# Kernel tuning notes

Measured on AMD Instinct MI355X. Metric: run time of the kernel, lower is better.

Reference implementation:

```python
import jax, jax.numpy as jnp
import numpy as np

B, H, S, D = 2, 16, 2048, 64

def setup_inputs() -> dict:
    key = jax.random.key(0)
    kq, kk, kv, km = jax.random.split(key, 4)
    q = jax.random.normal(kq, (B, H, S, D), dtype=jnp.float32)
    k = jax.random.normal(kk, (B, H, S, D), dtype=jnp.float32)
    v = jax.random.normal(kv, (B, H, S, D), dtype=jnp.float32)
    mask = jax.random.randint(km, (B, 1, S, S), 0, 2, dtype=jnp.int32)
    return {"q": q, "k": k, "v": v, "mask": mask}

def reference(q, k, v, mask):
    d_model = q.shape[-1]
    # scores: [B, H, S, S]
    score = jnp.einsum('bhqd,bhkd->bhqk', q, k) / jnp.sqrt(jnp.float32(d_model))
    score = jnp.where(mask == 0, jnp.float32(-1e9), score)
    attn = jax.nn.softmax(score, axis=-1)
    return jnp.einsum('bhqk,bhkd->bhqd', attn, v)
```

## Files before the change

### kernel.cpp

```cpp
#include <hip/hip_runtime.h>
#include <hip/hip_bf16.h>


#define B_ 2
#define H_ 16
#define S_ 2048
#define D_ 64
#define BQ 128
#define BK 64
#define NT (S_ / BK)
#define PADW 72
#define TILEB (BK * D_ * 2)

typedef __attribute__((ext_vector_type(4))) float f32x4;
typedef __attribute__((ext_vector_type(8))) short bf16x8;
typedef __attribute__((ext_vector_type(4))) short bf16x4;
typedef __attribute__((ext_vector_type(4))) unsigned u32x4;

#define QSCALE 0.1803368801111137f
#define MASKNEG (-1.4426950408889634e9f)

static __device__ __forceinline__ short f2bf(float f) {
  __hip_bfloat16 h = __float2bfloat16(f);
  short s; __builtin_memcpy(&s, &h, sizeof(s)); return s;
}
static __device__ __forceinline__ float fexp2(float x) {
  return __builtin_amdgcn_exp2f(x);
}
static __device__ __forceinline__ unsigned cvt_pk_bf16(float a, float b) {
  unsigned r;
  asm("v_cvt_pk_bf16_f32 %0, %1, %2" : "=v"(r) : "v"(a), "v"(b));
  return r;
}
static __device__ __forceinline__ void gload_lds16(const void* g, void* l) {
  __builtin_amdgcn_global_load_lds(
      (__attribute__((address_space(1))) void*)g,
      (__attribute__((address_space(3))) void*)l, 16, 0, 0);
}
static __device__ __forceinline__ void perm32sw(unsigned& a, unsigned& b) {
  asm("v_permlane32_swap_b32 %0, %1" : "+v"(a), "+v"(b));
}
static __device__ __forceinline__ void perm16sw(unsigned& a, unsigned& b) {
  asm("v_permlane16_swap_b32 %0, %1" : "+v"(a), "+v"(b));
}

__global__ __launch_bounds__(256)
void pack_all(const float* __restrict__ kg, const float* __restrict__ vg,
              const int* __restrict__ mg,
              short* __restrict__ kw, short* __restrict__ vw,
              unsigned long long* __restrict__ mwp) {
  __shared__ float sv[BK][D_ + 1];
  const int bx  = blockIdx.x;
  const int tid = threadIdx.x;

  if (bx < 1024) {
    const int t  = bx & 31;
    const int bh = bx >> 5;
    const float* kt = kg + ((size_t)bh * S_ + t * BK) * D_;
    const float* vt = vg + ((size_t)bh * S_ + t * BK) * D_;
    short* ko = kw + ((size_t)bh * NT + t) * (BK * D_);
    short* vo = vw + ((size_t)bh * NT + t) * (BK * D_);

    const int row = tid >> 2;
    const int swz = (row & 7) << 4;

    #pragma unroll
    for (int c = 0; c < 2; ++c) {
      const int x = (tid & 3) * 32 + c * 16;
      const int dsrc = (x ^ swz) >> 1;
      const float4 u0 = *(const float4*)(kt + row * D_ + dsrc);
      const float4 u1 = *(const float4*)(kt + row * D_ + dsrc + 4);
      uint4 w;
      w.x = cvt_pk_bf16(u0.x, u0.y); w.y = cvt_pk_bf16(u0.z, u0.w);
      w.z = cvt_pk_bf16(u1.x, u1.y); w.w = cvt_pk_bf16(u1.z, u1.w);
      *(uint4*)(ko + row * D_ + (x >> 1)) = w;
    }

    #pragma unroll
    for (int i = 0; i < 4; ++i) {
      const int id = tid + 256 * i;
      const int r = id >> 4, c4 = (id & 15) * 4;
      const float4 u = *(const float4*)(vt + r * D_ + c4);
      sv[r][c4] = u.x; sv[r][c4+1] = u.y; sv[r][c4+2] = u.z; sv[r][c4+3] = u.w;
    }
    __syncthreads();
    #pragma unroll
    for (int c = 0; c < 2; ++c) {
      const int x = (tid & 3) * 32 + c * 16;
      const int ksrc = (x ^ swz) >> 1;
      uint4 w;
      w.x = cvt_pk_bf16(sv[ksrc+0][row], sv[ksrc+1][row]);
      w.y = cvt_pk_bf16(sv[ksrc+2][row], sv[ksrc+3][row]);
      w.z = cvt_pk_bf16(sv[ksrc+4][row], sv[ksrc+5][row]);
      w.w = cvt_pk_bf16(sv[ksrc+6][row], sv[ksrc+7][row]);
      *(uint4*)(vo + row * D_ + (x >> 1)) = w;
    }
  } else {
    const int r4   = bx - 1024;
    const int wv   = tid >> 6;
    const int lane = tid & 63;
    const int row  = r4 * 4 + wv;
    const int* mr = mg + (size_t)row * S_;
    unsigned long long* out = mwp + (size_t)row * NT;
    #pragma unroll
    for (int g = 0; g < 8; ++g) {
      const int4 v = *(const int4*)(mr + g * 256 + lane * 4);
      const unsigned long long b0 = __ballot(v.x != 0);
      const unsigned long long b1 = __ballot(v.y != 0);
      const unsigned long long b2 = __ballot(v.z != 0);
      const unsigned long long b3 = __ballot(v.w != 0);
      if (lane < 4) {
        const int tl = lane;
        const unsigned long long u =
            ((b0 >> (16 * tl)) & 0xFFFFULL)
          | (((b1 >> (16 * tl)) & 0xFFFFULL) << 16)
          | (((b2 >> (16 * tl)) & 0xFFFFULL) << 32)
          | (((b3 >> (16 * tl)) & 0xFFFFULL) << 48);
        out[g * 4 + tl] = u;
      }
    }
  }
}

__global__ __launch_bounds__(512, 8)
void attn_main(const float* __restrict__ qg, const short* __restrict__ kw,
               const short* __restrict__ vw,
               const unsigned long long* __restrict__ mw,
               float* __restrict__ outg) {
  __shared__ short sKV[2][2][BK * D_];

  const int tid  = threadIdx.x;
  const int lane = tid & 63;
  const int wv   = tid >> 6;
  const int l15  = lane & 15;
  const int quad = lane >> 4;

  const int f  = blockIdx.y * 16 + blockIdx.x;
  const int nf = (f & 7) * 64 + (f >> 3);
  const int bh = nf >> 4;
  const int b  = bh >> 4;
  const int q0 = (nf & 15) * BQ;
  const int qw = q0 + wv * 16 + l15;

  bf16x8 qf[2];
  {
    const float* qrow = qg + ((size_t)bh * S_ + qw) * D_;
    #pragma unroll
    for (int ks = 0; ks < 2; ++ks) {
      const float4 u0 = *(const float4*)(qrow + ks*32 + quad*8);
      const float4 u1 = *(const float4*)(qrow + ks*32 + quad*8 + 4);
      bf16x8 fq;
      fq[0]=f2bf(u0.x*QSCALE); fq[1]=f2bf(u0.y*QSCALE);
      fq[2]=f2bf(u0.z*QSCALE); fq[3]=f2bf(u0.w*QSCALE);
      fq[4]=f2bf(u1.x*QSCALE); fq[5]=f2bf(u1.y*QSCALE);
      fq[6]=f2bf(u1.z*QSCALE); fq[7]=f2bf(u1.w*QSCALE);
      qf[ks] = fq;
    }
  }

  bf16x8 onesf;
  #pragma unroll
  for (int j = 0; j < 8; ++j) onesf[j] = (short)0x3F80;

  f32x4 O[4];
  #pragma unroll
  for (int dt = 0; dt < 4; ++dt) O[dt] = (f32x4){0.f, 0.f, 0.f, 0.f};
  f32x4 Ol = (f32x4){0.f, 0.f, 0.f, 0.f};

  const char* kt = (const char*)(kw + (size_t)bh * NT * BK * D_);
  const char* vt = (const char*)(vw + (size_t)bh * NT * BK * D_);
  const unsigned long long* mb = mw + ((size_t)b * S_ + qw) * NT;
  const int so = tid * 16;

  const int swz = (l15 & 7) << 4;
  const int ro0 = l15*128 + (( 0 + quad*16) ^ swz);
  const int ro1 = l15*128 + ((64 + quad*16) ^ swz);

  gload_lds16(kt + so, (char*)sKV + so);
  gload_lds16(vt + so, (char*)sKV + 8192 + so);
  kt += TILEB; vt += TILEB;
  int cur = 0;
  __syncthreads();

  for (int t = 0; t < NT; ++t) {
    const unsigned long long m64 = mb[t];
    if (t < NT - 1) {
      const int nb = (cur ^ 1) << 14;
      gload_lds16(kt + so, (char*)sKV + nb + so);
      gload_lds16(vt + so, (char*)sKV + nb + 8192 + so);
      kt += TILEB; vt += TILEB;
    }
    const char* kb = (const char*)sKV + (cur << 14);
    const char* vb = kb + 8192;

    f32x4 st[4];
    __builtin_amdgcn_s_setprio(1);
    #pragma unroll
    for (int mt = 0; mt < 4; ++mt) {
      f32x4 acc = (f32x4){0.f, 0.f, 0.f, 0.f};
      const bf16x8 kf0 = *(const bf16x8*)(kb + mt*2048 + ro0);
      const bf16x8 kf1 = *(const bf16x8*)(kb + mt*2048 + ro1);
      acc = __builtin_amdgcn_mfma_f32_16x16x32_bf16(kf0, qf[0], acc, 0, 0, 0);
      acc = __builtin_amdgcn_mfma_f32_16x16x32_bf16(kf1, qf[1], acc, 0, 0, 0);
      st[mt] = acc;
    }
    __builtin_amdgcn_s_setprio(0);

    const unsigned xlo = ((unsigned)m64) >> quad;
    const unsigned xhi = ((unsigned)(m64 >> 32)) >> quad;
    uint2 U[4];
    #pragma unroll
    for (int mt = 0; mt < 4; ++mt) {
      float p0 = fexp2(st[mt].x);
      float p1 = fexp2(st[mt].y);
      float p2 = fexp2(st[mt].z);
      float p3 = fexp2(st[mt].w);
      const int a0 = __builtin_amdgcn_sbfe((int)xlo, mt*4,      1);
      const int a1 = __builtin_amdgcn_sbfe((int)xlo, mt*4 + 16, 1);
      const int a2 = __builtin_amdgcn_sbfe((int)xhi, mt*4,      1);
      const int a3 = __builtin_amdgcn_sbfe((int)xhi, mt*4 + 16, 1);
      p0 = __uint_as_float(__float_as_uint(p0) & (unsigned)a0);
      p1 = __uint_as_float(__float_as_uint(p1) & (unsigned)a1);
      p2 = __uint_as_float(__float_as_uint(p2) & (unsigned)a2);
      p3 = __uint_as_float(__float_as_uint(p3) & (unsigned)a3);
      U[mt].x = cvt_pk_bf16(p0, p1);
      U[mt].y = cvt_pk_bf16(p2, p3);
    }

    unsigned w00 = U[0].x, w02 = U[1].x;
    perm32sw(w00, w02); perm16sw(w00, w02);
    unsigned w01 = U[0].y, w03 = U[1].y;
    perm32sw(w01, w03); perm16sw(w01, w03);
    unsigned w10 = U[2].x, w12 = U[3].x;
    perm32sw(w10, w12); perm16sw(w10, w12);
    unsigned w11 = U[2].y, w13 = U[3].y;
    perm32sw(w11, w13); perm16sw(w11, w13);
    bf16x8 pf0, pf1;
    {
      u32x4 t0 = (u32x4){w00, w01, w02, w03};
      u32x4 t1 = (u32x4){w10, w11, w12, w13};
      __builtin_memcpy(&pf0, &t0, 16);
      __builtin_memcpy(&pf1, &t1, 16);
    }

    __builtin_amdgcn_s_setprio(1);
    #pragma unroll
    for (int dt = 0; dt < 4; ++dt) {
      const bf16x8 vf0 = *(const bf16x8*)(vb + dt*2048 + ro0);
      const bf16x8 vf1 = *(const bf16x8*)(vb + dt*2048 + ro1);
      O[dt] = __builtin_amdgcn_mfma_f32_16x16x32_bf16(pf0, vf0, O[dt], 0, 0, 0);
      O[dt] = __builtin_amdgcn_mfma_f32_16x16x32_bf16(pf1, vf1, O[dt], 0, 0, 0);
    }
    Ol = __builtin_amdgcn_mfma_f32_16x16x32_bf16(pf0, onesf, Ol, 0, 0, 0);
    Ol = __builtin_amdgcn_mfma_f32_16x16x32_bf16(pf1, onesf, Ol, 0, 0, 0);
    __builtin_amdgcn_s_setprio(0);

    __syncthreads();
    cur ^= 1;
  }

  float ir[4];
  ir[0] = 1.0f / Ol.x; ir[1] = 1.0f / Ol.y;
  ir[2] = 1.0f / Ol.z; ir[3] = 1.0f / Ol.w;

  float* ob = outg + ((size_t)bh * S_ + q0 + wv*16) * D_;
  #pragma unroll
  for (int dt = 0; dt < 4; ++dt) {
    ob[(quad*4 + 0)*D_ + dt*16 + l15] = O[dt].x * ir[0];
    ob[(quad*4 + 1)*D_ + dt*16 + l15] = O[dt].y * ir[1];
    ob[(quad*4 + 2)*D_ + dt*16 + l15] = O[dt].z * ir[2];
    ob[(quad*4 + 3)*D_ + dt*16 + l15] = O[dt].w * ir[3];
  }
}

__global__ __launch_bounds__(256, 4)
void attn_fallback(const float* __restrict__ qg, const float* __restrict__ kg,
                   const float* __restrict__ vg, const int* __restrict__ maskg,
                   float* __restrict__ outg) {
  __shared__ short sK[BK][PADW];
  __shared__ short sVT[D_][PADW];
  __shared__ short sP[4][16][PADW];

  const int tid  = threadIdx.x;
  const int lane = tid & 63;
  const int wv   = tid >> 6;
  const int l15  = lane & 15;
  const int quad = lane >> 4;

  const int bh = blockIdx.y;
  const int b  = bh >> 4;
  const int q0 = blockIdx.x * 64;
  const int qw = q0 + wv * 16 + l15;

  bf16x8 qf[2];
  {
    const float* qrow = qg + ((size_t)bh * S_ + qw) * D_;
    #pragma unroll
    for (int ks = 0; ks < 2; ++ks) {
      const float4 u0 = *(const float4*)(qrow + ks*32 + quad*8);
      const float4 u1 = *(const float4*)(qrow + ks*32 + quad*8 + 4);
      bf16x8 fq;
      fq[0]=f2bf(u0.x*QSCALE); fq[1]=f2bf(u0.y*QSCALE);
      fq[2]=f2bf(u0.z*QSCALE); fq[3]=f2bf(u0.w*QSCALE);
      fq[4]=f2bf(u1.x*QSCALE); fq[5]=f2bf(u1.y*QSCALE);
      fq[6]=f2bf(u1.z*QSCALE); fq[7]=f2bf(u1.w*QSCALE);
      qf[ks] = fq;
    }
  }

  f32x4 O[4];
  #pragma unroll
  for (int dt = 0; dt < 4; ++dt) O[dt] = (f32x4){0.f, 0.f, 0.f, 0.f};
  float m = -3.0e38f, l = 0.f;

  const float* kbase = kg + (size_t)bh * S_ * D_;
  const float* vbase = vg + (size_t)bh * S_ * D_;
  const int*   mrow  = maskg + ((size_t)b * S_ + qw) * S_;

  for (int t0 = 0; t0 < S_; t0 += BK) {
    __syncthreads();
    #pragma unroll
    for (int i = 0; i < 4; ++i) {
      const int id = tid + 256*i;
      const int key = id >> 4, d4 = (id & 15) * 4;
      const float4 u = *(const float4*)(kbase + (size_t)(t0 + key)*D_ + d4);
      bf16x4 w; w[0]=f2bf(u.x); w[1]=f2bf(u.y); w[2]=f2bf(u.z); w[3]=f2bf(u.w);
      *(bf16x4*)&sK[key][d4] = w;
    }
    #pragma unroll
    for (int i = 0; i < 2; ++i) {
      const int id = tid + 256*i;
      const int kp = id & 31, d4 = (id >> 5) * 4;
      const float4 a = *(const float4*)(vbase + (size_t)(t0 + 2*kp    )*D_ + d4);
      const float4 c = *(const float4*)(vbase + (size_t)(t0 + 2*kp + 1)*D_ + d4);
      const float av[4] = {a.x, a.y, a.z, a.w};
      const float cv[4] = {c.x, c.y, c.z, c.w};
      #pragma unroll
      for (int j = 0; j < 4; ++j) {
        const unsigned pk = (unsigned)(unsigned short)f2bf(av[j])
                          | ((unsigned)(unsigned short)f2bf(cv[j]) << 16);
        *(unsigned*)&sVT[d4 + j][2*kp] = pk;
      }
    }
    __syncthreads();

    int4 mk[4];
    #pragma unroll
    for (int mt = 0; mt < 4; ++mt)
      mk[mt] = *(const int4*)(mrow + t0 + mt*16 + quad*4);

    f32x4 st[4];
    #pragma unroll
    for (int mt = 0; mt < 4; ++mt) {
      f32x4 acc = (f32x4){0.f, 0.f, 0.f, 0.f};
      #pragma unroll
      for (int ks = 0; ks < 2; ++ks) {
        const bf16x8 kf = *(const bf16x8*)&sK[mt*16 + l15][ks*32 + quad*8];
        acc = __builtin_amdgcn_mfma_f32_16x16x32_bf16(kf, qf[ks], acc, 0, 0, 0);
      }
      st[mt] = acc;
    }

    float cmax = -3.0e38f;
    #pragma unroll
    for (int mt = 0; mt < 4; ++mt) {
      f32x4 s = st[mt];
      s.x = mk[mt].x ? s.x : MASKNEG;
      s.y = mk[mt].y ? s.y : MASKNEG;
      s.z = mk[mt].z ? s.z : MASKNEG;
      s.w = mk[mt].w ? s.w : MASKNEG;
      st[mt] = s;
      cmax = fmaxf(cmax, fmaxf(fmaxf(s.x, s.y), fmaxf(s.z, s.w)));
    }
    cmax = fmaxf(cmax, __shfl_xor(cmax, 16));
    cmax = fmaxf(cmax, __shfl_xor(cmax, 32));
    const float mnew  = fmaxf(m, cmax);
    const float alpha = fexp2(m - mnew);
    m = mnew;

    float lsum = 0.f;
    #pragma unroll
    for (int mt = 0; mt < 4; ++mt) {
      const float p0 = fexp2(st[mt].x - mnew);
      const float p1 = fexp2(st[mt].y - mnew);
      const float p2 = fexp2(st[mt].z - mnew);
      const float p3 = fexp2(st[mt].w - mnew);
      lsum += (p0 + p1) + (p2 + p3);
      bf16x4 pw; pw[0]=f2bf(p0); pw[1]=f2bf(p1); pw[2]=f2bf(p2); pw[3]=f2bf(p3);
      *(bf16x4*)&sP[wv][l15][mt*16 + quad*4] = pw;
    }
    lsum += __shfl_xor(lsum, 16);
    lsum += __shfl_xor(lsum, 32);
    l = l * alpha + lsum;

    const float ar0 = __shfl(alpha, quad*4 + 0);
    const float ar1 = __shfl(alpha, quad*4 + 1);
    const float ar2 = __shfl(alpha, quad*4 + 2);
    const float ar3 = __shfl(alpha, quad*4 + 3);
    #pragma unroll
    for (int dt = 0; dt < 4; ++dt) {
      O[dt].x *= ar0; O[dt].y *= ar1; O[dt].z *= ar2; O[dt].w *= ar3;
    }

    asm volatile("s_waitcnt lgkmcnt(0)" ::: "memory");

    const bf16x8 pf0 = *(const bf16x8*)&sP[wv][l15][quad*8];
    const bf16x8 pf1 = *(const bf16x8*)&sP[wv][l15][32 + quad*8];
    #pragma unroll
    for (int dt = 0; dt < 4; ++dt) {
      const bf16x8 vf0 = *(const bf16x8*)&sVT[dt*16 + l15][quad*8];
      const bf16x8 vf1 = *(const bf16x8*)&sVT[dt*16 + l15][32 + quad*8];
      O[dt] = __builtin_amdgcn_mfma_f32_16x16x32_bf16(pf0, vf0, O[dt], 0, 0, 0);
      O[dt] = __builtin_amdgcn_mfma_f32_16x16x32_bf16(pf1, vf1, O[dt], 0, 0, 0);
    }
  }

  float ir[4];
  #pragma unroll
  for (int r = 0; r < 4; ++r) ir[r] = 1.0f / __shfl(l, quad*4 + r);

  float* ob = outg + ((size_t)bh * S_ + q0 + wv*16) * D_;
  #pragma unroll
  for (int dt = 0; dt < 4; ++dt) {
    ob[(quad*4 + 0)*D_ + dt*16 + l15] = O[dt].x * ir[0];
    ob[(quad*4 + 1)*D_ + dt*16 + l15] = O[dt].y * ir[1];
    ob[(quad*4 + 2)*D_ + dt*16 + l15] = O[dt].z * ir[2];
    ob[(quad*4 + 3)*D_ + dt*16 + l15] = O[dt].w * ir[3];
  }
}

extern "C" void kernel_launch(void* const* d_in, const int* in_sizes, int n_in,
                              void* d_out, int out_size, void* d_ws, size_t ws_size,
                              hipStream_t stream) {
  const float* q    = (const float*)d_in[0];
  const float* k    = (const float*)d_in[1];
  const float* v    = (const float*)d_in[2];
  const int*   mask = (const int*)d_in[3];
  float* out = (float*)d_out;

  const size_t kvbytes = (size_t)B_ * H_ * S_ * D_ * 2;
  const size_t mbytes  = (size_t)B_ * S_ * NT * 8;
  const size_t need    = 2 * kvbytes + mbytes;

  if (d_ws != nullptr && ws_size >= need) {
    short* kwp = (short*)d_ws;
    short* vwp = (short*)((char*)d_ws + kvbytes);
    unsigned long long* mwp = (unsigned long long*)((char*)d_ws + 2 * kvbytes);
    pack_all<<<dim3(2048), 256, 0, stream>>>(k, v, mask, kwp, vwp, mwp);
    attn_main<<<dim3(S_ / BQ, B_ * H_), 512, 0, stream>>>(q, kwp, vwp, mwp, out);
  } else {
    attn_fallback<<<dim3(S_ / 64, B_ * H_), 256, 0, stream>>>(q, k, v, mask, out);
  }
}
```

Baseline: 169.5 us.

## Split KV range across two blocks and combine partial outputs

```diff
diff --git a/kernel.cpp b/kernel.cpp
--- a/kernel.cpp
+++ b/kernel.cpp
@@ -9,6 +9,7 @@
 #define BQ 128
 #define BK 64
 #define NT (S_ / BK)
+#define NTH (NT / 2)
 #define PADW 72
 #define TILEB (BK * D_ * 2)
 
@@ -123,10 +124,10 @@
 }
 
 __global__ __launch_bounds__(512, 8)
-void attn_main(const float* __restrict__ qg, const short* __restrict__ kw,
-               const short* __restrict__ vw,
-               const unsigned long long* __restrict__ mw,
-               float* __restrict__ outg) {
+void attn_split(const float* __restrict__ qg, const short* __restrict__ kw,
+                const short* __restrict__ vw,
+                const unsigned long long* __restrict__ mw,
+                float* __restrict__ Op, float* __restrict__ lw) {
   __shared__ short sKV[2][2][BK * D_];
 
   const int tid  = threadIdx.x;
@@ -135,12 +136,16 @@
   const int l15  = lane & 15;
   const int quad = lane >> 4;
 
-  const int f  = blockIdx.y * 16 + blockIdx.x;
-  const int nf = (f & 7) * 64 + (f >> 3);
-  const int bh = nf >> 4;
+  const int f  = blockIdx.y * 32 + blockIdx.x;
+  const int nf = (f & 7) * 128 + (f >> 3);
+  const int bh = nf >> 5;
   const int b  = bh >> 4;
-  const int q0 = (nf & 15) * BQ;
+  const int rest = nf & 31;
+  const int qb = rest >> 1;
+  const int sp = rest & 1;
+  const int q0 = qb * BQ;
   const int qw = q0 + wv * 16 + l15;
+  const int soff = sp * NTH;
 
   bf16x8 qf[2];
   {
@@ -167,9 +172,9 @@
   for (int dt = 0; dt < 4; ++dt) O[dt] = (f32x4){0.f, 0.f, 0.f, 0.f};
   f32x4 Ol = (f32x4){0.f, 0.f, 0.f, 0.f};
 
-  const char* kt = (const char*)(kw + (size_t)bh * NT * BK * D_);
-  const char* vt = (const char*)(vw + (size_t)bh * NT * BK * D_);
-  const unsigned long long* mb = mw + ((size_t)b * S_ + qw) * NT;
+  const char* kt = (const char*)(kw + ((size_t)bh * NT + soff) * BK * D_);
+  const char* vt = (const char*)(vw + ((size_t)bh * NT + soff) * BK * D_);
+  const unsigned long long* mb = mw + ((size_t)b * S_ + qw) * NT + soff;
   const int so = tid * 16;
 
   const int swz = (l15 & 7) << 4;
@@ -182,9 +187,9 @@
   int cur = 0;
   __syncthreads();
 
-  for (int t = 0; t < NT; ++t) {
+  for (int t = 0; t < NTH; ++t) {
     const unsigned long long m64 = mb[t];
-    if (t < NT - 1) {
+    if (t < NTH - 1) {
       const int nb = (cur ^ 1) << 14;
       gload_lds16(kt + so, (char*)sKV + nb + so);
       gload_lds16(vt + so, (char*)sKV + nb + 8192 + so);
@@ -259,6 +264,174 @@
     cur ^= 1;
   }
 
+  float* ob = Op + (((size_t)sp * 32 + bh) * S_ + q0 + wv*16) * D_;
+  #pragma unroll
+  for (int dt = 0; dt < 4; ++dt) {
+    ob[(quad*4 + 0)*D_ + dt*16 + l15] = O[dt].x;
+    ob[(quad*4 + 1)*D_ + dt*16 + l15] = O[dt].y;
+    ob[(quad*4 + 2)*D_ + dt*16 + l15] = O[dt].z;
+    ob[(quad*4 + 3)*D_ + dt*16 + l15] = O[dt].w;
+  }
+  if (l15 == 0) {
+    float* lb = lw + ((size_t)sp * 32 + bh) * S_ + q0 + wv*16 + quad*4;
+    lb[0] = Ol.x; lb[1] = Ol.y; lb[2] = Ol.z; lb[3] = Ol.w;
+  }
+}
+
+__global__ __launch_bounds__(256)
+void combine(const float* __restrict__ Op, const float* __restrict__ lw,
+             float* __restrict__ outg) {
+  const size_t OPHALF = (size_t)32 * S_ * D_;
+  const size_t LHALF  = (size_t)32 * S_;
+  const int gid = blockIdx.x * 256 + threadIdx.x;
+  const int r  = gid >> 4;
+  const int d4 = (gid & 15) * 4;
+  const float4 a = *(const float4*)(Op + (size_t)r * D_ + d4);
+  const float4 c = *(const float4*)(Op + OPHALF + (size_t)r * D_ + d4);
+  const float li = 1.0f / (lw[r] + lw[LHALF + r]);
+  float4 o;
+  o.x = (a.x + c.x) * li; o.y = (a.y + c.y) * li;
+  o.z = (a.z + c.z) * li; o.w = (a.w + c.w) * li;
+  *(float4*)(outg + (size_t)r * D_ + d4) = o;
+}
+
+__global__ __launch_bounds__(512, 8)
+void attn_main(const float* __restrict__ qg, const short* __restrict__ kw,
+               const short* __restrict__ vw,
+               const unsigned long long* __restrict__ mw,
+               float* __restrict__ outg) {
+  __shared__ short sKV[2][2][BK * D_];
+
+  const int tid  = threadIdx.x;
+  const int lane = tid & 63;
+  const int wv   = tid >> 6;
+  const int l15  = lane & 15;
+  const int quad = lane >> 4;
+
+  const int f  = blockIdx.y * 16 + blockIdx.x;
+  const int nf = (f & 7) * 64 + (f >> 3);
+  const int bh = nf >> 4;
+  const int b  = bh >> 4;
+  const int q0 = (nf & 15) * BQ;
+  const int qw = q0 + wv * 16 + l15;
+
+  bf16x8 qf[2];
+  {
+    const float* qrow = qg + ((size_t)bh * S_ + qw) * D_;
+    #pragma unroll
+    for (int ks = 0; ks < 2; ++ks) {
+      const float4 u0 = *(const float4*)(qrow + ks*32 + quad*8);
+      const float4 u1 = *(const float4*)(qrow + ks*32 + quad*8 + 4);
+      bf16x8 fq;
+      fq[0]=f2bf(u0.x*QSCALE); fq[1]=f2bf(u0.y*QSCALE);
+      fq[2]=f2bf(u0.z*QSCALE); fq[3]=f2bf(u0.w*QSCALE);
+      fq[4]=f2bf(u1.x*QSCALE); fq[5]=f2bf(u1.y*QSCALE);
+      fq[6]=f2bf(u1.z*QSCALE); fq[7]=f2bf(u1.w*QSCALE);
+      qf[ks] = fq;
+    }
+  }
+
+  bf16x8 onesf;
+  #pragma unroll
+  for (int j = 0; j < 8; ++j) onesf[j] = (short)0x3F80;
+
+  f32x4 O[4];
+  #pragma unroll
+  for (int dt = 0; dt < 4; ++dt) O[dt] = (f32x4){0.f, 0.f, 0.f, 0.f};
+  f32x4 Ol = (f32x4){0.f, 0.f, 0.f, 0.f};
+
+  const char* kt = (const char*)(kw + (size_t)bh * NT * BK * D_);
+  const char* vt = (const char*)(vw + (size_t)bh * NT * BK * D_);
+  const unsigned long long* mb = mw + ((size_t)b * S_ + qw) * NT;
+  const int so = tid * 16;
+
+  const int swz = (l15 & 7) << 4;
+  const int ro0 = l15*128 + (( 0 + quad*16) ^ swz);
+  const int ro1 = l15*128 + ((64 + quad*16) ^ swz);
+
+  gload_lds16(kt + so, (char*)sKV + so);
+  gload_lds16(vt + so, (char*)sKV + 8192 + so);
+  kt += TILEB; vt += TILEB;
+  int cur = 0;
+  __syncthreads();
+
+  for (int t = 0; t < NT; ++t) {
+    const unsigned long long m64 = mb[t];
+    if (t < NT - 1) {
+      const int nb = (cur ^ 1) << 14;
+      gload_lds16(kt + so, (char*)sKV + nb + so);
+      gload_lds16(vt + so, (char*)sKV + nb + 8192 + so);
+      kt += TILEB; vt += TILEB;
+    }
+    const char* kb = (const char*)sKV + (cur << 14);
+    const char* vb = kb + 8192;
+
+    f32x4 st[4];
+    __builtin_amdgcn_s_setprio(1);
+    #pragma unroll
+    for (int mt = 0; mt < 4; ++mt) {
+      f32x4 acc = (f32x4){0.f, 0.f, 0.f, 0.f};
+      const bf16x8 kf0 = *(const bf16x8*)(kb + mt*2048 + ro0);
+      const bf16x8 kf1 = *(const bf16x8*)(kb + mt*2048 + ro1);
+      acc = __builtin_amdgcn_mfma_f32_16x16x32_bf16(kf0, qf[0], acc, 0, 0, 0);
+      acc = __builtin_amdgcn_mfma_f32_16x16x32_bf16(kf1, qf[1], acc, 0, 0, 0);
+      st[mt] = acc;
+    }
+    __builtin_amdgcn_s_setprio(0);
+
+    const unsigned xlo = ((unsigned)m64) >> quad;
+    const unsigned xhi = ((unsigned)(m64 >> 32)) >> quad;
+    uint2 U[4];
+    #pragma unroll
+    for (int mt = 0; mt < 4; ++mt) {
+      float p0 = fexp2(st[mt].x);
+      float p1 = fexp2(st[mt].y);
+      float p2 = fexp2(st[mt].z);
+      float p3 = fexp2(st[mt].w);
+      const int a0 = __builtin_amdgcn_sbfe((int)xlo, mt*4,      1);
+      const int a1 = __builtin_amdgcn_sbfe((int)xlo, mt*4 + 16, 1);
+      const int a2 = __builtin_amdgcn_sbfe((int)xhi, mt*4,      1);
+      const int a3 = __builtin_amdgcn_sbfe((int)xhi, mt*4 + 16, 1);
+      p0 = __uint_as_float(__float_as_uint(p0) & (unsigned)a0);
+      p1 = __uint_as_float(__float_as_uint(p1) & (unsigned)a1);
+      p2 = __uint_as_float(__float_as_uint(p2) & (unsigned)a2);
+      p3 = __uint_as_float(__float_as_uint(p3) & (unsigned)a3);
+      U[mt].x = cvt_pk_bf16(p0, p1);
+      U[mt].y = cvt_pk_bf16(p2, p3);
+    }
+
+    unsigned w00 = U[0].x, w02 = U[1].x;
+    perm32sw(w00, w02); perm16sw(w00, w02);
+    unsigned w01 = U[0].y, w03 = U[1].y;
+    perm32sw(w01, w03); perm16sw(w01, w03);
+    unsigned w10 = U[2].x, w12 = U[3].x;
+    perm32sw(w10, w12); perm16sw(w10, w12);
+    unsigned w11 = U[2].y, w13 = U[3].y;
+    perm32sw(w11, w13); perm16sw(w11, w13);
+    bf16x8 pf0, pf1;
+    {
+      u32x4 t0 = (u32x4){w00, w01, w02, w03};
+      u32x4 t1 = (u32x4){w10, w11, w12, w13};
+      __builtin_memcpy(&pf0, &t0, 16);
+      __builtin_memcpy(&pf1, &t1, 16);
+    }
+
+    __builtin_amdgcn_s_setprio(1);
+    #pragma unroll
+    for (int dt = 0; dt < 4; ++dt) {
+      const bf16x8 vf0 = *(const bf16x8*)(vb + dt*2048 + ro0);
+      const bf16x8 vf1 = *(const bf16x8*)(vb + dt*2048 + ro1);
+      O[dt] = __builtin_amdgcn_mfma_f32_16x16x32_bf16(pf0, vf0, O[dt], 0, 0, 0);
+      O[dt] = __builtin_amdgcn_mfma_f32_16x16x32_bf16(pf1, vf1, O[dt], 0, 0, 0);
+    }
+    Ol = __builtin_amdgcn_mfma_f32_16x16x32_bf16(pf0, onesf, Ol, 0, 0, 0);
+    Ol = __builtin_amdgcn_mfma_f32_16x16x32_bf16(pf1, onesf, Ol, 0, 0, 0);
+    __builtin_amdgcn_s_setprio(0);
+
+    __syncthreads();
+    cur ^= 1;
+  }
+
   float ir[4];
   ir[0] = 1.0f / Ol.x; ir[1] = 1.0f / Ol.y;
   ir[2] = 1.0f / Ol.z; ir[3] = 1.0f / Ol.w;
@@ -440,14 +613,24 @@
 
   const size_t kvbytes = (size_t)B_ * H_ * S_ * D_ * 2;
   const size_t mbytes  = (size_t)B_ * S_ * NT * 8;
-  const size_t need    = 2 * kvbytes + mbytes;
-
-  if (d_ws != nullptr && ws_size >= need) {
+  const size_t opbytes = (size_t)2 * 32 * S_ * D_ * 4;
+  const size_t lbytes  = (size_t)2 * 32 * S_ * 4;
+  const size_t need_base  = 2 * kvbytes + mbytes;
+  const size_t need_split = need_base + opbytes + lbytes;
+
+  if (d_ws != nullptr && ws_size >= need_base) {
     short* kwp = (short*)d_ws;
     short* vwp = (short*)((char*)d_ws + kvbytes);
     unsigned long long* mwp = (unsigned long long*)((char*)d_ws + 2 * kvbytes);
     pack_all<<<dim3(2048), 256, 0, stream>>>(k, v, mask, kwp, vwp, mwp);
-    attn_main<<<dim3(S_ / BQ, B_ * H_), 512, 0, stream>>>(q, kwp, vwp, mwp, out);
+    if (ws_size >= need_split) {
+      float* opp = (float*)((char*)d_ws + need_base);
+      float* lwp = (float*)((char*)d_ws + need_base + opbytes);
+      attn_split<<<dim3(32, 32), 512, 0, stream>>>(q, kwp, vwp, mwp, opp, lwp);
+      combine<<<dim3((32 * S_ * 16) / 256), 256, 0, stream>>>(opp, lwp, out);
+    } else {
+      attn_main<<<dim3(16, 32), 512, 0, stream>>>(q, kwp, vwp, mwp, out);
+    }
   } else {
     attn_fallback<<<dim3(S_ / 64, B_ * H_), 256, 0, stream>>>(q, k, v, mask, out);
   }
```

After: 171.9 us. About the same (+1.4%).
